# Kernel tuning notes

Hardware: AMD Instinct MI355X
Metric: run time of the kernel (lower is better)

Reference implementation:

```python
import jax, jax.numpy as jnp
import numpy as np


def _unpack_int4(w_i32):
    # w_i32: [N, K//8] int32, 8 signed int4 nibbles per int32 (low nibble first)
    shifts = jnp.arange(8, dtype=jnp.int32) * 4
    nib = (w_i32[:, :, None] >> shifts[None, None, :]) & 0xF  # [N, K//8, 8]
    signed = (nib ^ 8) - 8  # map [0,15] -> [-8,7]
    N = w_i32.shape[0]
    return signed.reshape(N, -1)  # [N, K] int32 in [-8,7]


def setup_inputs() -> dict:
    key = jax.random.key(0)
    k1, k2, k3, k4, k5 = jax.random.split(key, 5)
    M, K, N, G = 4096, 4096, 14336, 128
    qx = jax.random.normal(k1, (M, K), dtype=jnp.float32)
    qxscale = jax.random.uniform(k2, (M, 1), dtype=jnp.float32, minval=0.5, maxval=1.5)
    weight_i4 = jax.random.randint(k3, (N, K // 8), 0, 2147483647, dtype=jnp.int32)
    weight_scale = jax.random.uniform(k4, (N, K // G), dtype=jnp.float32, minval=0.001, maxval=0.02)
    bias = jax.random.normal(k5, (N,), dtype=jnp.float32) * 0.02
    return {"qx": qx, "qxscale": qxscale, "weight_i4": weight_i4,
            "weight_scale": weight_scale, "bias": bias, "group_size": G}


def reference(qx, qxscale, weight_i4, weight_scale, bias, group_size):
    # 1) unpack int32 -> int4  2) per-group dequant  3) matmul  4) scale+bias  5) silu
    iweight = _unpack_int4(weight_i4)  # [N, K]
    N, K = iweight.shape
    deq_w = (iweight.astype(jnp.float32).reshape(N, K // group_size, group_size)
             * weight_scale[:, :, None]).reshape(N, K)  # [N, K]
    y = jnp.einsum('mk,nk->mn', qx, deq_w) * qxscale  # [M, N]
    y = y + bias[None, :]
    return jax.nn.silu(y)
```

## Files before the change

### kernel.cpp

```cpp
#include <hip/hip_runtime.h>
#include <hip/hip_bf16.h>
#include <stdint.h>


#define M_DIM 4096
#define K_DIM 4096
#define N_DIM 14336
#define GSZ   128

typedef __bf16 bf16x8 __attribute__((ext_vector_type(8)));
typedef __bf16 bf16x4 __attribute__((ext_vector_type(4)));
typedef float  f32x4  __attribute__((ext_vector_type(4)));

#define GLOAD16(g, l) __builtin_amdgcn_global_load_lds( \
    (const __attribute__((address_space(1))) void*)(g), \
    (__attribute__((address_space(3))) void*)(l), 16, 0, 0)

#define WAITVM(N) asm volatile("s_waitcnt vmcnt(" #N ")" ::: "memory")


__global__ __launch_bounds__(256) void convertA_kernel(
    const float* __restrict__ qx, __bf16* __restrict__ out)
{
    const size_t i = ((size_t)blockIdx.x * 256 + threadIdx.x) * 8;
    const float4 a = *(const float4*)(qx + i);
    const float4 b = *(const float4*)(qx + i + 4);
    bf16x8 v;
    v[0] = (__bf16)a.x; v[1] = (__bf16)a.y; v[2] = (__bf16)a.z; v[3] = (__bf16)a.w;
    v[4] = (__bf16)b.x; v[5] = (__bf16)b.y; v[6] = (__bf16)b.z; v[7] = (__bf16)b.w;
    *(bf16x8*)(out + i) = v;
}

__global__ __launch_bounds__(256) void dequantW_kernel(
    const int* __restrict__ wq, const float* __restrict__ wscale,
    __bf16* __restrict__ out)
{
    const size_t g = (size_t)blockIdx.x * 256 + threadIdx.x;
    const int n  = (int)(g >> 9);
    const int wi = (int)(g & 511);
    const float s = wscale[(size_t)n * (K_DIM / GSZ) + (wi >> 4)];
    const int w = wq[g];
    bf16x8 v;
    #pragma unroll
    for (int j = 0; j < 8; ++j) {
        const int q = ((int)((unsigned)w << (28 - 4 * j))) >> 28;
        v[j] = (__bf16)((float)q * s);
    }
    *(bf16x8*)(out + g * 8) = v;
}


constexpr int BM = 256, BN = 256, BK = 32;
constexpr int NT = K_DIM / BK;
constexpr int BUF_BYTES = 32768;

__global__ __launch_bounds__(512, 2) void gemm256_kernel(
    const __bf16* __restrict__ A,
    const __bf16* __restrict__ B,
    const float* __restrict__ qxscale,
    const float* __restrict__ bias,
    float* __restrict__ out)
{
    __shared__ __align__(16) char smem[4 * BUF_BYTES];

    const int t    = threadIdx.x;
    const int lane = t & 63;
    const int wave = t >> 6;
    const int wr   = wave >> 2;
    const int wc   = wave & 3;

    const int bid = blockIdx.x;
    const int cpx = (M_DIM / BM) * (N_DIM / BN) / 8;
    const int wg  = (bid & 7) * cpx + (bid >> 3);
    const int tiles_n = N_DIM / BN;
    const int tm = wg / tiles_n, tn = wg % tiles_n;
    const int m0 = tm * BM, n0 = tn * BN;

    const int srow = t >> 2;
    const int scb  = ((t & 3) * 16) ^ (((t >> 3) & 3) << 4);
    const char* aS = (const char*)A + (size_t)(m0 + srow) * K_DIM * 2 + scb;
    const char* bS = (const char*)B + (size_t)(n0 + srow) * K_DIM * 2 + scb;
    const size_t sweepG = (size_t)128 * K_DIM * 2;
    char* sbase = smem;

    auto STAGE_A = [&](int kt) {
        char* d = sbase + (kt & 3) * BUF_BYTES + t * 16;
        const char* s = aS + (size_t)kt * 64;
        GLOAD16(s, d);
        GLOAD16(s + sweepG, d + 8192);
    };
    auto STAGE_B = [&](int kt) {
        char* d = sbase + (kt & 3) * BUF_BYTES + 16384 + t * 16;
        const char* s = bS + (size_t)kt * 64;
        GLOAD16(s, d);
        GLOAD16(s + sweepG, d + 8192);
    };

    const int lane15 = lane & 15;
    const int pkb = ((lane >> 4) * 16) ^ (((lane >> 1) & 3) << 4);
    const int aRowB = (wr * 128 + lane15) * 64 + pkb;
    const int bRowB = (wc * 64 + lane15) * 64 + pkb + 16384;

    f32x4 acc[8][4] = {};

    STAGE_A(0); STAGE_B(0);
    STAGE_A(1); STAGE_B(1);
    STAGE_A(2); STAGE_B(2);
    WAITVM(8);
    __builtin_amdgcn_s_barrier();
    __builtin_amdgcn_sched_barrier(0);

    for (int kt = 0; kt < NT; ++kt) {
        const char* buf = sbase + (kt & 3) * BUF_BYTES;
        bf16x8 af[8], bf[4];

        #pragma unroll
        for (int ni = 0; ni < 4; ++ni)
            bf[ni] = *(const bf16x8*)(buf + bRowB + ni * 1024);
        #pragma unroll
        for (int mi = 0; mi < 8; ++mi)
            af[mi] = *(const bf16x8*)(buf + aRowB + mi * 1024);

        if (kt + 3 < NT) { STAGE_A(kt + 3); STAGE_B(kt + 3); }

        __builtin_amdgcn_s_setprio(1);
        #pragma unroll
        for (int mi = 0; mi < 8; ++mi)
            #pragma unroll
            for (int ni = 0; ni < 4; ++ni)
                acc[mi][ni] = __builtin_amdgcn_mfma_f32_16x16x32_bf16(
                    af[mi], bf[ni], acc[mi][ni], 0, 0, 0);
        __builtin_amdgcn_s_setprio(0);

        if (kt + 1 < NT) {
            if (kt + 3 < NT)      WAITVM(8);
            else if (kt + 2 < NT) WAITVM(4);
            else                  WAITVM(0);
            __builtin_amdgcn_s_barrier();
            __builtin_amdgcn_sched_barrier(0);
        }
    }

    const int c_col = lane & 15;
    const int c_r4  = (lane >> 4) * 4;
    #pragma unroll
    for (int mi = 0; mi < 8; ++mi) {
        const int mg = m0 + wr * 128 + mi * 16 + c_r4;
        float qs[4];
        #pragma unroll
        for (int r = 0; r < 4; ++r) qs[r] = qxscale[mg + r];
        #pragma unroll
        for (int ni = 0; ni < 4; ++ni) {
            const int ng = n0 + wc * 64 + ni * 16 + c_col;
            const float bv = bias[ng];
            #pragma unroll
            for (int r = 0; r < 4; ++r) {
                const float y = acc[mi][ni][r] * qs[r] + bv;
                out[(size_t)(mg + r) * N_DIM + ng] = y / (1.f + __expf(-y));
            }
        }
    }
}


constexpr int FBM = 128, FBN = 128, FBK = 64;
constexpr int FLDA = 72;

__global__ __launch_bounds__(256) void gateproj_fused_kernel(
    const float* __restrict__ qx, const float* __restrict__ qxscale,
    const int* __restrict__ wq, const float* __restrict__ wscale,
    const float* __restrict__ bias, float* __restrict__ out)
{
    __shared__ __bf16 sA[FBM * FLDA];
    __shared__ __bf16 sB[FBN * FLDA];

    const int tid  = threadIdx.x;
    const int lane = tid & 63;
    const int wave = tid >> 6;
    const int wm = wave >> 1, wn = wave & 1;

    const int bid = blockIdx.x;
    const int cpx = (M_DIM / FBM) * (N_DIM / FBN) / 8;
    const int wg  = (bid & 7) * cpx + (bid >> 3);
    const int tiles_n = N_DIM / FBN;
    const int tm = wg / tiles_n, tn = wg % tiles_n;
    const int m0 = tm * FBM, n0 = tn * FBN;

    const int a_row = tid >> 4;
    const int a_col = (tid & 15) * 4;
    const float* aPtr = qx + (size_t)(m0 + a_row) * K_DIM + a_col;

    const int b_row = tid >> 1;
    const int b_wb  = (tid & 1) * 4;
    const int*   bPtr = wq     + (size_t)(n0 + b_row) * (K_DIM / 8) + b_wb;
    const float* sPtr = wscale + (size_t)(n0 + b_row) * (K_DIM / GSZ);

    float4 aReg[8];
    int    bRegW[4];
    float  bScl;
    f32x4 acc[4][4] = {};

    auto LOAD = [&](int kt) {
        const float* ap = aPtr + kt * FBK;
        #pragma unroll
        for (int i = 0; i < 8; ++i)
            aReg[i] = *(const float4*)(ap + (size_t)i * 16 * K_DIM);
        int4 b = *(const int4*)(bPtr + kt * 8);
        bRegW[0] = b.x; bRegW[1] = b.y; bRegW[2] = b.z; bRegW[3] = b.w;
        bScl = sPtr[kt >> 1];
    };

    auto STORE = [&]() {
        #pragma unroll
        for (int i = 0; i < 8; ++i) {
            bf16x4 v;
            v[0] = (__bf16)aReg[i].x; v[1] = (__bf16)aReg[i].y;
            v[2] = (__bf16)aReg[i].z; v[3] = (__bf16)aReg[i].w;
            *(bf16x4*)&sA[(a_row + i * 16) * FLDA + a_col] = v;
        }
        const int cb = (tid & 1) * 32;
        #pragma unroll
        for (int wi = 0; wi < 4; ++wi) {
            const int w = bRegW[wi];
            bf16x8 o;
            #pragma unroll
            for (int j = 0; j < 8; ++j) {
                const int v = ((int)((unsigned)w << (28 - 4 * j))) >> 28;
                o[j] = (__bf16)((float)v * bScl);
            }
            *(bf16x8*)&sB[b_row * FLDA + cb + wi * 8] = o;
        }
    };

    LOAD(0); STORE(); __syncthreads();

    const int FNT = K_DIM / FBK;
    for (int kt = 0; kt < FNT; ++kt) {
        if (kt + 1 < FNT) LOAD(kt + 1);
        #pragma unroll
        for (int kk = 0; kk < 2; ++kk) {
            bf16x8 af[4], bfr[4];
            const int ko = kk * 32 + (lane >> 4) * 8;
            #pragma unroll
            for (int mi = 0; mi < 4; ++mi)
                af[mi] = *(const bf16x8*)&sA[(wm * 64 + mi * 16 + (lane & 15)) * FLDA + ko];
            #pragma unroll
            for (int ni = 0; ni < 4; ++ni)
                bfr[ni] = *(const bf16x8*)&sB[(wn * 64 + ni * 16 + (lane & 15)) * FLDA + ko];
            #pragma unroll
            for (int mi = 0; mi < 4; ++mi)
                #pragma unroll
                for (int ni = 0; ni < 4; ++ni)
                    acc[mi][ni] = __builtin_amdgcn_mfma_f32_16x16x32_bf16(
                        af[mi], bfr[ni], acc[mi][ni], 0, 0, 0);
        }
        __syncthreads();
        if (kt + 1 < FNT) { STORE(); __syncthreads(); }
    }

    const int c_col = lane & 15;
    const int c_r4  = (lane >> 4) * 4;
    #pragma unroll
    for (int mi = 0; mi < 4; ++mi) {
        const int mg = m0 + wm * 64 + mi * 16 + c_r4;
        float qs[4];
        #pragma unroll
        for (int r = 0; r < 4; ++r) qs[r] = qxscale[mg + r];
        #pragma unroll
        for (int ni = 0; ni < 4; ++ni) {
            const int ng = n0 + wn * 64 + ni * 16 + c_col;
            const float bv = bias[ng];
            #pragma unroll
            for (int r = 0; r < 4; ++r) {
                const float y = acc[mi][ni][r] * qs[r] + bv;
                out[(size_t)(mg + r) * N_DIM + ng] = y / (1.f + __expf(-y));
            }
        }
    }
}


extern "C" void kernel_launch(void* const* d_in, const int* in_sizes, int n_in,
                              void* d_out, int out_size, void* d_ws, size_t ws_size,
                              hipStream_t stream) {
    const float* qx      = (const float*)d_in[0];
    const float* qxscale = (const float*)d_in[1];
    const int*   wq      = (const int*)d_in[2];
    const float* wscale  = (const float*)d_in[3];
    const float* bias    = (const float*)d_in[4];
    float* out = (float*)d_out;

    const size_t needA = (size_t)M_DIM * K_DIM * 2;
    const size_t needW = (size_t)N_DIM * K_DIM * 2;

    if (ws_size >= needA + needW) {
        __bf16* Abf = (__bf16*)d_ws;
        __bf16* Wbf = Abf + (size_t)M_DIM * K_DIM;

        hipLaunchKernelGGL(convertA_kernel, dim3(M_DIM * K_DIM / 8 / 256), dim3(256),
                           0, stream, qx, Abf);
        hipLaunchKernelGGL(dequantW_kernel, dim3(N_DIM * (K_DIM / 8) / 256), dim3(256),
                           0, stream, wq, wscale, Wbf);

        const int grid = (M_DIM / BM) * (N_DIM / BN);
        hipLaunchKernelGGL(gemm256_kernel, dim3(grid), dim3(512), 0, stream,
                           Abf, Wbf, qxscale, bias, out);
    } else {
        const int grid = (M_DIM / FBM) * (N_DIM / FBN);
        hipLaunchKernelGGL(gateproj_fused_kernel, dim3(grid), dim3(256), 0, stream,
                           qx, qxscale, wq, wscale, bias, out);
    }
}
```

Before: 526.9 us.

## Restructure GEMM main loop into 8-phase ping-pong schedule with BK=64

Doubles the K tile to 64 with two 64KB LDS buffers and splits each tile's work into four quadrant phases. Each phase interleaves LDS fragment reads and quarter-tile global-to-LDS prefetches with a block of MFMAs, separated by barriers and priority toggles. A new XOR swizzle matches the 128-byte rows. The aim is to overlap memory traffic with matrix math and cut the number of loop iterations and barriers per K element, at the cost of more barriers per tile, larger LDS use that may limit occupancy, and more complex wait-count bookkeeping.

```diff
diff --git a/kernel.cpp b/kernel.cpp
--- a/kernel.cpp
+++ b/kernel.cpp
@@ -17,6 +17,7 @@
     (__attribute__((address_space(3))) void*)(l), 16, 0, 0)
 
 #define WAITVM(N) asm volatile("s_waitcnt vmcnt(" #N ")" ::: "memory")
+#define WAITLGKM0() asm volatile("s_waitcnt lgkmcnt(0)" ::: "memory")
 
 
 __global__ __launch_bounds__(256) void convertA_kernel(
@@ -50,9 +51,10 @@
 }
 
 
-constexpr int BM = 256, BN = 256, BK = 32;
-constexpr int NT = K_DIM / BK;
-constexpr int BUF_BYTES = 32768;
+constexpr int BM = 256, BN = 256, BK = 64;
+constexpr int NT  = K_DIM / BK;
+constexpr int NIT = NT / 2;
+constexpr int BUF_BYTES = 65536;
 
 __global__ __launch_bounds__(512, 2) void gemm256_kernel(
     const __bf16* __restrict__ A,
@@ -61,7 +63,7 @@
     const float* __restrict__ bias,
     float* __restrict__ out)
 {
-    __shared__ __align__(16) char smem[4 * BUF_BYTES];
+    __shared__ __align__(16) char smem[2 * BUF_BYTES];
 
     const int t    = threadIdx.x;
     const int lane = t & 63;
@@ -76,70 +78,139 @@
     const int tm = wg / tiles_n, tn = wg % tiles_n;
     const int m0 = tm * BM, n0 = tn * BN;
 
-    const int srow = t >> 2;
-    const int scb  = ((t & 3) * 16) ^ (((t >> 3) & 3) << 4);
-    const char* aS = (const char*)A + (size_t)(m0 + srow) * K_DIM * 2 + scb;
-    const char* bS = (const char*)B + (size_t)(n0 + srow) * K_DIM * 2 + scb;
-    const size_t sweepG = (size_t)128 * K_DIM * 2;
+    const int srow = t >> 3;
+    const int sg16 = (((t & 7) ^ (srow & 7)) << 4);
+    const size_t KB = (size_t)K_DIM * 2;
+    const char* aS = (const char*)A + (size_t)(m0 + srow) * KB + sg16;
+    const char* bS = (const char*)B + (size_t)(n0 + srow) * KB + sg16;
     char* sbase = smem;
 
-    auto STAGE_A = [&](int kt) {
-        char* d = sbase + (kt & 3) * BUF_BYTES + t * 16;
-        const char* s = aS + (size_t)kt * 64;
-        GLOAD16(s, d);
-        GLOAD16(s + sweepG, d + 8192);
-    };
-    auto STAGE_B = [&](int kt) {
-        char* d = sbase + (kt & 3) * BUF_BYTES + 16384 + t * 16;
-        const char* s = bS + (size_t)kt * 64;
-        GLOAD16(s, d);
-        GLOAD16(s + sweepG, d + 8192);
+    auto STAGE_AQ = [&](int tile, int q) {
+        GLOAD16(aS + (size_t)tile * 128 + (size_t)q * 64 * KB,
+                sbase + (tile & 1) * BUF_BYTES + q * 8192 + t * 16);
+    };
+    auto STAGE_BQ = [&](int tile, int q) {
+        GLOAD16(bS + (size_t)tile * 128 + (size_t)q * 64 * KB,
+                sbase + (tile & 1) * BUF_BYTES + 32768 + q * 8192 + t * 16);
     };
 
     const int lane15 = lane & 15;
-    const int pkb = ((lane >> 4) * 16) ^ (((lane >> 1) & 3) << 4);
-    const int aRowB = (wr * 128 + lane15) * 64 + pkb;
-    const int bRowB = (wc * 64 + lane15) * 64 + pkb + 16384;
+    const int lc     = lane >> 4;
+    const int swzc   = ((lc ^ (lane15 & 7)) << 4);
+    const int aR0 = (wr * 128 + lane15) * 128 + swzc;
+    const int aR1 = aR0 ^ 64;
+    const int bR0 = 32768 + (wc * 64 + lane15) * 128 + swzc;
+    const int bR1 = bR0 ^ 64;
 
     f32x4 acc[8][4] = {};
-
-    STAGE_A(0); STAGE_B(0);
-    STAGE_A(1); STAGE_B(1);
-    STAGE_A(2); STAGE_B(2);
-    WAITVM(8);
+    bf16x8 af[4][2], bfl[2][2], bfh[2][2];
+
+    auto DS_AF = [&](const char* buf, int mibase) {
+        #pragma unroll
+        for (int mi = 0; mi < 4; ++mi) {
+            af[mi][0] = *(const bf16x8*)(buf + aR0 + (mibase + mi) * 2048);
+            af[mi][1] = *(const bf16x8*)(buf + aR1 + (mibase + mi) * 2048);
+        }
+    };
+    auto DS_BL = [&](const char* buf) {
+        #pragma unroll
+        for (int ni = 0; ni < 2; ++ni) {
+            bfl[ni][0] = *(const bf16x8*)(buf + bR0 + ni * 2048);
+            bfl[ni][1] = *(const bf16x8*)(buf + bR1 + ni * 2048);
+        }
+    };
+    auto DS_BH = [&](const char* buf) {
+        #pragma unroll
+        for (int ni = 0; ni < 2; ++ni) {
+            bfh[ni][0] = *(const bf16x8*)(buf + bR0 + (2 + ni) * 2048);
+            bfh[ni][1] = *(const bf16x8*)(buf + bR1 + (2 + ni) * 2048);
+        }
+    };
+    auto MFMAQ_L = [&](int mo) {
+        #pragma unroll
+        for (int kk = 0; kk < 2; ++kk)
+            #pragma unroll
+            for (int mi = 0; mi < 4; ++mi)
+                #pragma unroll
+                for (int ni = 0; ni < 2; ++ni)
+                    acc[mo + mi][ni] = __builtin_amdgcn_mfma_f32_16x16x32_bf16(
+                        af[mi][kk], bfl[ni][kk], acc[mo + mi][ni], 0, 0, 0);
+    };
+    auto MFMAQ_H = [&](int mo) {
+        #pragma unroll
+        for (int kk = 0; kk < 2; ++kk)
+            #pragma unroll
+            for (int mi = 0; mi < 4; ++mi)
+                #pragma unroll
+                for (int ni = 0; ni < 2; ++ni)
+                    acc[mo + mi][2 + ni] = __builtin_amdgcn_mfma_f32_16x16x32_bf16(
+                        af[mi][kk], bfh[ni][kk], acc[mo + mi][2 + ni], 0, 0, 0);
+    };
+
+    #define PH_SYNC() do { __builtin_amdgcn_s_barrier(); WAITLGKM0(); \
+        __builtin_amdgcn_sched_barrier(0); __builtin_amdgcn_s_setprio(1); } while (0)
+    #define PH_END() do { __builtin_amdgcn_s_setprio(0); \
+        __builtin_amdgcn_s_barrier(); } while (0)
+
+    #pragma unroll
+    for (int q = 0; q < 4; ++q) STAGE_AQ(0, q);
+    #pragma unroll
+    for (int q = 0; q < 4; ++q) STAGE_BQ(0, q);
+    STAGE_AQ(1, 0); STAGE_AQ(1, 2);
+    #pragma unroll
+    for (int q = 0; q < 4; ++q) STAGE_BQ(1, q);
+    WAITVM(6);
     __builtin_amdgcn_s_barrier();
     __builtin_amdgcn_sched_barrier(0);
 
-    for (int kt = 0; kt < NT; ++kt) {
-        const char* buf = sbase + (kt & 3) * BUF_BYTES;
-        bf16x8 af[8], bf[4];
-
-        #pragma unroll
-        for (int ni = 0; ni < 4; ++ni)
-            bf[ni] = *(const bf16x8*)(buf + bRowB + ni * 1024);
-        #pragma unroll
-        for (int mi = 0; mi < 8; ++mi)
-            af[mi] = *(const bf16x8*)(buf + aRowB + mi * 1024);
-
-        if (kt + 3 < NT) { STAGE_A(kt + 3); STAGE_B(kt + 3); }
-
+    for (int i = 0; i < NIT; ++i) {
+        const int t0 = 2 * i, t1 = 2 * i + 1;
+        const bool more = (i + 1 < NIT);
+        const char* bufE = sbase;
+        const char* bufO = sbase + BUF_BYTES;
+
+        DS_AF(bufE, 0); DS_BL(bufE);
+        STAGE_AQ(t1, 1); STAGE_AQ(t1, 3);
+        PH_SYNC(); MFMAQ_L(0); PH_END();
+
+        DS_BH(bufE);
+        if (more) { STAGE_AQ(t0 + 2, 0); STAGE_AQ(t0 + 2, 2); }
+        PH_SYNC(); MFMAQ_H(0); PH_END();
+
+        DS_AF(bufE, 4);
+        if (more) { STAGE_BQ(t0 + 2, 0); STAGE_BQ(t0 + 2, 1); }
+        PH_SYNC(); MFMAQ_H(4); PH_END();
+
+        if (more) { STAGE_BQ(t0 + 2, 2); STAGE_BQ(t0 + 2, 3); WAITVM(6); }
+        else      { WAITVM(0); }
+        __builtin_amdgcn_s_barrier();
+        __builtin_amdgcn_sched_barrier(0);
         __builtin_amdgcn_s_setprio(1);
-        #pragma unroll
-        for (int mi = 0; mi < 8; ++mi)
-            #pragma unroll
-            for (int ni = 0; ni < 4; ++ni)
-                acc[mi][ni] = __builtin_amdgcn_mfma_f32_16x16x32_bf16(
-                    af[mi], bf[ni], acc[mi][ni], 0, 0, 0);
-        __builtin_amdgcn_s_setprio(0);
-
-        if (kt + 1 < NT) {
-            if (kt + 3 < NT)      WAITVM(8);
-            else if (kt + 2 < NT) WAITVM(4);
-            else                  WAITVM(0);
-            __builtin_amdgcn_s_barrier();
-            __builtin_amdgcn_sched_barrier(0);
-        }
-    }
+        MFMAQ_L(4);
+        PH_END();
+
+        DS_AF(bufO, 0); DS_BL(bufO);
+        if (more) { STAGE_AQ(t0 + 2, 1); STAGE_AQ(t0 + 2, 3); }
+        PH_SYNC(); MFMAQ_L(0); PH_END();
+
+        DS_BH(bufO);
+        if (more) { STAGE_AQ(t1 + 2, 0); STAGE_AQ(t1 + 2, 2); }
+        PH_SYNC(); MFMAQ_H(0); PH_END();
+
+        DS_AF(bufO, 4);
+        if (more) { STAGE_BQ(t1 + 2, 0); STAGE_BQ(t1 + 2, 1); }
+        PH_SYNC(); MFMAQ_H(4); PH_END();
+
+        if (more) { STAGE_BQ(t1 + 2, 2); STAGE_BQ(t1 + 2, 3); WAITVM(6); }
+        __builtin_amdgcn_s_barrier();
+        __builtin_amdgcn_sched_barrier(0);
+        __builtin_amdgcn_s_setprio(1);
+        MFMAQ_L(4);
+        PH_END();
+    }
+
+    #undef PH_SYNC
+    #undef PH_END
 
     const int c_col = lane & 15;
     const int c_r4  = (lane >> 4) * 4;
```

Measured after the change: 502.8 us. 4.6% less time.

## Restructure bf16 GEMM to 128x256x64 tiles with double-buffered split-MFMA pipeline

Applied to the files above, without the earlier changes.

Replaces the 256x256x32 four-stage GEMM with a 128x256 tile using BK=64, two LDS buffers, and a new XOR swizzle. Each K tile is processed in two MFMA halves so that global-to-LDS staging of the next tile is issued between them, with explicit lgkmcnt/vmcnt waits and barriers. The smaller M tile halves the accumulator registers and doubles the grid. In exchange it lowers arithmetic intensity per block, which raises operand traffic, and adds extra barriers per K tile.

```diff
diff --git a/kernel.cpp b/kernel.cpp
--- a/kernel.cpp
+++ b/kernel.cpp
@@ -17,6 +17,7 @@
     (__attribute__((address_space(3))) void*)(l), 16, 0, 0)
 
 #define WAITVM(N) asm volatile("s_waitcnt vmcnt(" #N ")" ::: "memory")
+#define WAITLGKM(N) asm volatile("s_waitcnt lgkmcnt(" #N ")" ::: "memory")
 
 
 __global__ __launch_bounds__(256) void convertA_kernel(
@@ -50,18 +51,19 @@
 }
 
 
-constexpr int BM = 256, BN = 256, BK = 32;
-constexpr int NT = K_DIM / BK;
-constexpr int BUF_BYTES = 32768;
-
-__global__ __launch_bounds__(512, 2) void gemm256_kernel(
+constexpr int BM = 128, BN = 256, BK = 64;
+constexpr int NT  = K_DIM / BK;
+constexpr int NIT = NT / 2;
+constexpr int BUF_BYTES = 49152;
+
+__global__ __launch_bounds__(512, 2) void gemm128_kernel(
     const __bf16* __restrict__ A,
     const __bf16* __restrict__ B,
     const float* __restrict__ qxscale,
     const float* __restrict__ bias,
     float* __restrict__ out)
 {
-    __shared__ __align__(16) char smem[4 * BUF_BYTES];
+    __shared__ __align__(16) char smem[2 * BUF_BYTES];
 
     const int t    = threadIdx.x;
     const int lane = t & 63;
@@ -76,66 +78,102 @@
     const int tm = wg / tiles_n, tn = wg % tiles_n;
     const int m0 = tm * BM, n0 = tn * BN;
 
-    const int srow = t >> 2;
-    const int scb  = ((t & 3) * 16) ^ (((t >> 3) & 3) << 4);
-    const char* aS = (const char*)A + (size_t)(m0 + srow) * K_DIM * 2 + scb;
-    const char* bS = (const char*)B + (size_t)(n0 + srow) * K_DIM * 2 + scb;
-    const size_t sweepG = (size_t)128 * K_DIM * 2;
+    const int srow = t >> 3;
+    const int sg16 = (((t & 7) ^ (srow & 7)) << 4);
+    const size_t KB = (size_t)K_DIM * 2;
+    const char* aS = (const char*)A + (size_t)(m0 + srow) * KB + sg16;
+    const char* bS = (const char*)B + (size_t)(n0 + srow) * KB + sg16;
     char* sbase = smem;
 
-    auto STAGE_A = [&](int kt) {
-        char* d = sbase + (kt & 3) * BUF_BYTES + t * 16;
-        const char* s = aS + (size_t)kt * 64;
-        GLOAD16(s, d);
-        GLOAD16(s + sweepG, d + 8192);
-    };
-    auto STAGE_B = [&](int kt) {
-        char* d = sbase + (kt & 3) * BUF_BYTES + 16384 + t * 16;
-        const char* s = bS + (size_t)kt * 64;
-        GLOAD16(s, d);
-        GLOAD16(s + sweepG, d + 8192);
+    auto STAGE_A = [&](int tile, int q) {
+        GLOAD16(aS + (size_t)tile * 128 + (size_t)q * 64 * KB,
+                sbase + (tile & 1) * BUF_BYTES + q * 8192 + t * 16);
+    };
+    auto STAGE_B = [&](int tile, int q) {
+        GLOAD16(bS + (size_t)tile * 128 + (size_t)q * 64 * KB,
+                sbase + (tile & 1) * BUF_BYTES + 16384 + q * 8192 + t * 16);
+    };
+    auto STAGE_ALL = [&](int tile) {
+        STAGE_A(tile, 0); STAGE_A(tile, 1);
+        STAGE_B(tile, 0); STAGE_B(tile, 1);
+        STAGE_B(tile, 2); STAGE_B(tile, 3);
     };
 
     const int lane15 = lane & 15;
-    const int pkb = ((lane >> 4) * 16) ^ (((lane >> 1) & 3) << 4);
-    const int aRowB = (wr * 128 + lane15) * 64 + pkb;
-    const int bRowB = (wc * 64 + lane15) * 64 + pkb + 16384;
-
-    f32x4 acc[8][4] = {};
-
-    STAGE_A(0); STAGE_B(0);
-    STAGE_A(1); STAGE_B(1);
-    STAGE_A(2); STAGE_B(2);
-    WAITVM(8);
+    const int lc     = lane >> 4;
+    const int swzc   = ((lc ^ (lane15 & 7)) << 4);
+    const int aR0 = (wr * 64 + lane15) * 128 + swzc;
+    const int bR0 = 16384 + (wc * 64 + lane15) * 128 + swzc;
+
+    f32x4 acc[4][4] = {};
+    bf16x8 af[4][2], bfr[4][2];
+
+    auto DS_TILE = [&](const char* buf) {
+        #pragma unroll
+        for (int mi = 0; mi < 4; ++mi) {
+            const int a0 = aR0 + mi * 2048;
+            af[mi][0] = *(const bf16x8*)(buf + a0);
+            af[mi][1] = *(const bf16x8*)(buf + (a0 ^ 64));
+        }
+        #pragma unroll
+        for (int ni = 0; ni < 4; ++ni) {
+            const int b0 = bR0 + ni * 2048;
+            bfr[ni][0] = *(const bf16x8*)(buf + b0);
+            bfr[ni][1] = *(const bf16x8*)(buf + (b0 ^ 64));
+        }
+    };
+    auto MFMA_HALF = [&](int nb) {
+        #pragma unroll
+        for (int kk = 0; kk < 2; ++kk)
+            #pragma unroll
+            for (int mi = 0; mi < 4; ++mi)
+                #pragma unroll
+                for (int ni = 0; ni < 2; ++ni)
+                    acc[mi][nb + ni] = __builtin_amdgcn_mfma_f32_16x16x32_bf16(
+                        af[mi][kk], bfr[nb + ni][kk], acc[mi][nb + ni], 0, 0, 0);
+    };
+
+    STAGE_ALL(0); STAGE_ALL(1);
+    WAITVM(6);
     __builtin_amdgcn_s_barrier();
     __builtin_amdgcn_sched_barrier(0);
 
-    for (int kt = 0; kt < NT; ++kt) {
-        const char* buf = sbase + (kt & 3) * BUF_BYTES;
-        bf16x8 af[8], bf[4];
-
-        #pragma unroll
-        for (int ni = 0; ni < 4; ++ni)
-            bf[ni] = *(const bf16x8*)(buf + bRowB + ni * 1024);
-        #pragma unroll
-        for (int mi = 0; mi < 8; ++mi)
-            af[mi] = *(const bf16x8*)(buf + aRowB + mi * 1024);
-
-        if (kt + 3 < NT) { STAGE_A(kt + 3); STAGE_B(kt + 3); }
-
+    for (int i = 0; i < NIT; ++i) {
+        const int t0 = 2 * i, t1 = 2 * i + 1;
+        const bool more = (i + 1 < NIT);
+        const char* bufE = sbase;
+        const char* bufO = sbase + BUF_BYTES;
+
+        DS_TILE(bufE);
+        WAITLGKM(4);
+        __builtin_amdgcn_sched_barrier(0);
         __builtin_amdgcn_s_setprio(1);
-        #pragma unroll
-        for (int mi = 0; mi < 8; ++mi)
-            #pragma unroll
-            for (int ni = 0; ni < 4; ++ni)
-                acc[mi][ni] = __builtin_amdgcn_mfma_f32_16x16x32_bf16(
-                    af[mi], bf[ni], acc[mi][ni], 0, 0, 0);
+        MFMA_HALF(0);
         __builtin_amdgcn_s_setprio(0);
-
-        if (kt + 1 < NT) {
-            if (kt + 3 < NT)      WAITVM(8);
-            else if (kt + 2 < NT) WAITVM(4);
-            else                  WAITVM(0);
+        __builtin_amdgcn_s_barrier();
+
+        if (more) STAGE_ALL(t0 + 2);
+        __builtin_amdgcn_s_setprio(1);
+        MFMA_HALF(2);
+        __builtin_amdgcn_s_setprio(0);
+        if (more) WAITVM(6); else WAITVM(0);
+        __builtin_amdgcn_s_barrier();
+        __builtin_amdgcn_sched_barrier(0);
+
+        DS_TILE(bufO);
+        WAITLGKM(4);
+        __builtin_amdgcn_sched_barrier(0);
+        __builtin_amdgcn_s_setprio(1);
+        MFMA_HALF(0);
+        __builtin_amdgcn_s_setprio(0);
+        __builtin_amdgcn_s_barrier();
+
+        if (more) STAGE_ALL(t1 + 2);
+        __builtin_amdgcn_s_setprio(1);
+        MFMA_HALF(2);
+        __builtin_amdgcn_s_setprio(0);
+        if (more) {
+            WAITVM(6);
             __builtin_amdgcn_s_barrier();
             __builtin_amdgcn_sched_barrier(0);
         }
@@ -144,8 +182,8 @@
     const int c_col = lane & 15;
     const int c_r4  = (lane >> 4) * 4;
     #pragma unroll
-    for (int mi = 0; mi < 8; ++mi) {
-        const int mg = m0 + wr * 128 + mi * 16 + c_r4;
+    for (int mi = 0; mi < 4; ++mi) {
+        const int mg = m0 + wr * 64 + mi * 16 + c_r4;
         float qs[4];
         #pragma unroll
         for (int r = 0; r < 4; ++r) qs[r] = qxscale[mg + r];
@@ -239,20 +277,20 @@
         if (kt + 1 < FNT) LOAD(kt + 1);
         #pragma unroll
         for (int kk = 0; kk < 2; ++kk) {
-            bf16x8 af[4], bfr[4];
+            bf16x8 af2[4], bfr2[4];
             const int ko = kk * 32 + (lane >> 4) * 8;
             #pragma unroll
             for (int mi = 0; mi < 4; ++mi)
-                af[mi] = *(const bf16x8*)&sA[(wm * 64 + mi * 16 + (lane & 15)) * FLDA + ko];
+                af2[mi] = *(const bf16x8*)&sA[(wm * 64 + mi * 16 + (lane & 15)) * FLDA + ko];
             #pragma unroll
             for (int ni = 0; ni < 4; ++ni)
-                bfr[ni] = *(const bf16x8*)&sB[(wn * 64 + ni * 16 + (lane & 15)) * FLDA + ko];
+                bfr2[ni] = *(const bf16x8*)&sB[(wn * 64 + ni * 16 + (lane & 15)) * FLDA + ko];
             #pragma unroll
             for (int mi = 0; mi < 4; ++mi)
                 #pragma unroll
                 for (int ni = 0; ni < 4; ++ni)
                     acc[mi][ni] = __builtin_amdgcn_mfma_f32_16x16x32_bf16(
-                        af[mi], bfr[ni], acc[mi][ni], 0, 0, 0);
+                        af2[mi], bfr2[ni], acc[mi][ni], 0, 0, 0);
         }
         __syncthreads();
         if (kt + 1 < FNT) { STORE(); __syncthreads(); }
@@ -303,7 +341,7 @@
                            0, stream, wq, wscale, Wbf);
 
         const int grid = (M_DIM / BM) * (N_DIM / BN);
-        hipLaunchKernelGGL(gemm256_kernel, dim3(grid), dim3(512), 0, stream,
+        hipLaunchKernelGGL(gemm128_kernel, dim3(grid), dim3(512), 0, stream,
                            Abf, Wbf, qxscale, bias, out);
     } else {
         const int grid = (M_DIM / FBM) * (N_DIM / FBN);
```

Measured after the change: 619.9 us. +17.6%, slower.

## Software-pipeline LDS fragment reads against MFMA in main GEMM loop

Applied to the files above, without the earlier changes.

Restructures the main bf16 GEMM loop into a manually unrolled two-step pipeline. It prefetches A/B fragments for the next k-tile from LDS into double-buffered registers while MFMAs for the current half-tile run, using explicit lgkmcnt waits and sched barriers. The global-to-LDS wait depth is also tightened to one outstanding stage, since reading next-tile LDS early needs that buffer ready. The aim is to hide LDS read latency behind matrix math, at the cost of more VGPRs and a tighter dependency on the async copy finishing sooner.

```diff
diff --git a/kernel.cpp b/kernel.cpp
--- a/kernel.cpp
+++ b/kernel.cpp
@@ -17,6 +17,8 @@
     (__attribute__((address_space(3))) void*)(l), 16, 0, 0)
 
 #define WAITVM(N) asm volatile("s_waitcnt vmcnt(" #N ")" ::: "memory")
+#define WAITLGKM(N) asm volatile("s_waitcnt lgkmcnt(" #N ")" ::: "memory")
+#define SB0() __builtin_amdgcn_sched_barrier(0)
 
 
 __global__ __launch_bounds__(256) void convertA_kernel(
@@ -102,44 +104,90 @@
     const int bRowB = (wc * 64 + lane15) * 64 + pkb + 16384;
 
     f32x4 acc[8][4] = {};
+    bf16x8 afc[4], bfc[4];
+    bf16x8 afn[4], bfn[4];
+    bf16x8 af1[4];
+
+    #define LA4(BUF, AF, BASE) do { _Pragma("unroll") \
+        for (int i_ = 0; i_ < 4; ++i_) \
+            AF[i_] = *(const bf16x8*)((BUF) + aRowB + ((BASE) + i_) * 1024); \
+        } while (0)
+    #define LB4(BUF, BF) do { _Pragma("unroll") \
+        for (int n_ = 0; n_ < 4; ++n_) \
+            BF[n_] = *(const bf16x8*)((BUF) + bRowB + n_ * 1024); \
+        } while (0)
+    #define MM16(AF, BF, AB) do { _Pragma("unroll") \
+        for (int mi_ = 0; mi_ < 4; ++mi_) { _Pragma("unroll") \
+            for (int ni_ = 0; ni_ < 4; ++ni_) \
+                acc[(AB) + mi_][ni_] = __builtin_amdgcn_mfma_f32_16x16x32_bf16( \
+                    AF[mi_], BF[ni_], acc[(AB) + mi_][ni_], 0, 0, 0); } \
+        } while (0)
 
     STAGE_A(0); STAGE_B(0);
     STAGE_A(1); STAGE_B(1);
     STAGE_A(2); STAGE_B(2);
-    WAITVM(8);
+    WAITVM(4);
     __builtin_amdgcn_s_barrier();
-    __builtin_amdgcn_sched_barrier(0);
-
-    for (int kt = 0; kt < NT; ++kt) {
-        const char* buf = sbase + (kt & 3) * BUF_BYTES;
-        bf16x8 af[8], bf[4];
-
-        #pragma unroll
-        for (int ni = 0; ni < 4; ++ni)
-            bf[ni] = *(const bf16x8*)(buf + bRowB + ni * 1024);
-        #pragma unroll
-        for (int mi = 0; mi < 8; ++mi)
-            af[mi] = *(const bf16x8*)(buf + aRowB + mi * 1024);
-
-        if (kt + 3 < NT) { STAGE_A(kt + 3); STAGE_B(kt + 3); }
-
-        __builtin_amdgcn_s_setprio(1);
-        #pragma unroll
-        for (int mi = 0; mi < 8; ++mi)
-            #pragma unroll
-            for (int ni = 0; ni < 4; ++ni)
-                acc[mi][ni] = __builtin_amdgcn_mfma_f32_16x16x32_bf16(
-                    af[mi], bf[ni], acc[mi][ni], 0, 0, 0);
-        __builtin_amdgcn_s_setprio(0);
-
-        if (kt + 1 < NT) {
-            if (kt + 3 < NT)      WAITVM(8);
-            else if (kt + 2 < NT) WAITVM(4);
-            else                  WAITVM(0);
+    SB0();
+    LA4(sbase, afc, 0);
+    LB4(sbase, bfc);
+
+    for (int it = 0; it < NT / 2; ++it) {
+        {
+            const int kt = 2 * it;
+            const char* buf = sbase + (kt & 3) * BUF_BYTES;
+            LA4(buf, af1, 4);
+            if (kt + 3 < NT) { STAGE_A(kt + 3); STAGE_B(kt + 3); }
+            WAITLGKM(4);
+            SB0();
+            __builtin_amdgcn_s_setprio(1);
+            MM16(afc, bfc, 0);
+            __builtin_amdgcn_s_setprio(0);
+            {
+                const char* nb = sbase + ((kt + 1) & 3) * BUF_BYTES;
+                LA4(nb, afn, 0);
+                LB4(nb, bfn);
+            }
+            WAITLGKM(8);
+            SB0();
+            __builtin_amdgcn_s_setprio(1);
+            MM16(af1, bfc, 4);
+            __builtin_amdgcn_s_setprio(0);
+            if (kt + 3 < NT) WAITVM(4); else WAITVM(0);
             __builtin_amdgcn_s_barrier();
-            __builtin_amdgcn_sched_barrier(0);
-        }
-    }
+            SB0();
+        }
+        {
+            const int kt = 2 * it + 1;
+            const char* buf = sbase + (kt & 3) * BUF_BYTES;
+            LA4(buf, af1, 4);
+            if (kt + 3 < NT) { STAGE_A(kt + 3); STAGE_B(kt + 3); }
+            WAITLGKM(4);
+            SB0();
+            __builtin_amdgcn_s_setprio(1);
+            MM16(afn, bfn, 0);
+            __builtin_amdgcn_s_setprio(0);
+            if (kt + 1 < NT) {
+                const char* nb = sbase + ((kt + 1) & 3) * BUF_BYTES;
+                LA4(nb, afc, 0);
+                LB4(nb, bfc);
+                WAITLGKM(8);
+            } else {
+                WAITLGKM(0);
+            }
+            SB0();
+            __builtin_amdgcn_s_setprio(1);
+            MM16(af1, bfn, 4);
+            __builtin_amdgcn_s_setprio(0);
+            if (kt + 3 < NT) WAITVM(4); else WAITVM(0);
+            __builtin_amdgcn_s_barrier();
+            SB0();
+        }
+    }
+
+    #undef LA4
+    #undef LB4
+    #undef MM16
 
     const int c_col = lane & 15;
     const int c_r4  = (lane >> 4) * 4;
@@ -239,20 +287,20 @@
         if (kt + 1 < FNT) LOAD(kt + 1);
         #pragma unroll
         for (int kk = 0; kk < 2; ++kk) {
-            bf16x8 af[4], bfr[4];
+            bf16x8 af2[4], bfr2[4];
             const int ko = kk * 32 + (lane >> 4) * 8;
             #pragma unroll
             for (int mi = 0; mi < 4; ++mi)
-                af[mi] = *(const bf16x8*)&sA[(wm * 64 + mi * 16 + (lane & 15)) * FLDA + ko];
+                af2[mi] = *(const bf16x8*)&sA[(wm * 64 + mi * 16 + (lane & 15)) * FLDA + ko];
             #pragma unroll
             for (int ni = 0; ni < 4; ++ni)
-                bfr[ni] = *(const bf16x8*)&sB[(wn * 64 + ni * 16 + (lane & 15)) * FLDA + ko];
+                bfr2[ni] = *(const bf16x8*)&sB[(wn * 64 + ni * 16 + (lane & 15)) * FLDA + ko];
             #pragma unroll
             for (int mi = 0; mi < 4; ++mi)
                 #pragma unroll
                 for (int ni = 0; ni < 4; ++ni)
                     acc[mi][ni] = __builtin_amdgcn_mfma_f32_16x16x32_bf16(
-                        af[mi], bfr[ni], acc[mi][ni], 0, 0, 0);
+                        af2[mi], bfr2[ni], acc[mi][ni], 0, 0, 0);
         }
         __syncthreads();
         if (kt + 1 < FNT) { STORE(); __syncthreads(); }
```

Result: faster. 510.5 us (-3.1%).
